# Performance work log

Hardware: AMD Instinct MI355X
Metric: run time of the kernel (lower is better)

Reference implementation:

```python
import jax, jax.numpy as jnp
import numpy as np

N_NODES = 100000
N_EDGES = 1600000
C = 64


def _spline_conv(x, src, dst, u, w, root, bias, n_nodes):
    """SplineConv, dim=1, kernel_size=2, degree=1, open spline, aggr='mean'.

    For K=2, degree=1, pseudo u in [0,1]: basis = (1-u) on knot 0, u on knot 1.
    message_e = (1-u_e) * x[src_e] @ w[0] + u_e * x[src_e] @ w[1]
    Compute the two GEMMs at node level (N < E) then gather, which is
    mathematically identical and cheaper.
    """
    h0 = x @ w[0]  # [N, C]
    h1 = x @ w[1]  # [N, C]
    uc = u[:, None]  # [E, 1]
    msg = (1.0 - uc) * h0[src] + uc * h1[src]  # [E, C]
    agg = jax.ops.segment_sum(msg, dst, num_segments=n_nodes)  # [N, C]
    deg = jax.ops.segment_sum(jnp.ones_like(u), dst, num_segments=n_nodes)
    agg = agg / jnp.maximum(deg, 1.0)[:, None]  # mean aggregation
    return agg + x @ root + bias


def setup_inputs() -> dict:
    key = jax.random.key(0)
    ks = jax.random.split(key, 10)
    x = jax.random.normal(ks[0], (N_NODES, C), dtype=jnp.float32)
    edge_index = jax.random.randint(ks[1], (2, N_EDGES), 0, N_NODES, dtype=jnp.int64)
    edge_attr = jax.random.uniform(ks[2], (N_EDGES, 1), dtype=jnp.float32)
    s = 1.0 / np.sqrt(C)
    w1 = jax.random.uniform(ks[3], (2, C, C), jnp.float32, -s, s)
    root1 = jax.random.uniform(ks[4], (C, C), jnp.float32, -s, s)
    b1 = jnp.zeros((C,), jnp.float32)
    w2 = jax.random.uniform(ks[5], (2, C, C), jnp.float32, -s, s)
    root2 = jax.random.uniform(ks[6], (C, C), jnp.float32, -s, s)
    b2 = jnp.zeros((C,), jnp.float32)
    return {"x": x, "edge_index": edge_index, "edge_attr": edge_attr,
            "w1": w1, "root1": root1, "b1": b1,
            "w2": w2, "root2": root2, "b2": b2}


def reference(x, edge_index, edge_attr, w1, root1, b1, w2, root2, b2):
    src, dst = edge_index[0], edge_index[1]
    u = edge_attr[:, 0]
    n = x.shape[0]
    h = _spline_conv(x, src, dst, u, w1, root1, b1, n)
    h = _spline_conv(h, src, dst, u, w2, root2, b2, n)
    return h
```

## Files before the change

### kernel.cpp

```cpp
#include <hip/hip_runtime.h>

#define CDIM 64

typedef __attribute__((ext_vector_type(8))) short bf16x8;
typedef __attribute__((ext_vector_type(4))) float f32x4;

__device__ __forceinline__ short bf16r(float f) {
    unsigned a = __float_as_uint(f);
    a = (a + 0x7fffu + ((a >> 16) & 1u)) >> 16;
    return (short)a;
}
__device__ __forceinline__ unsigned bfpack(float lo, float hi) {
    unsigned a = __float_as_uint(lo);
    a = (a + 0x7fffu + ((a >> 16) & 1u)) >> 16;
    unsigned b = __float_as_uint(hi);
    b = (b + 0x7fffu + ((b >> 16) & 1u)) & 0xffff0000u;
    return a | b;
}

__global__ __launch_bounds__(256) void k_pack(const float* __restrict__ x,
                                              unsigned* __restrict__ xb32, size_t n2) {
    size_t t = (size_t)blockIdx.x * 256 + threadIdx.x;
    size_t stride = (size_t)gridDim.x * 256;
    for (size_t i = t; i < n2; i += stride) {
        float2 v = ((const float2*)x)[i];
        xb32[i] = bfpack(v.x, v.y);
    }
}

#define NPB_SHIFT 9
#define BKN (1 << NPB_SHIFT)
#define BPAD 10240
#define PART_CH 2048

__global__ __launch_bounds__(256) void k_prep(int* __restrict__ bkt_cursor, int n_buckets,
                                              const float* __restrict__ w1,
                                              const float* __restrict__ root1,
                                              const float* __restrict__ w2,
                                              const float* __restrict__ root2,
                                              short* __restrict__ wtg) {
    int tid = threadIdx.x;
    if (blockIdx.x == 0) {
        if (tid < n_buckets) bkt_cursor[tid] = tid * BPAD;
        return;
    }
    int l = blockIdx.x - 1;
    const float* s0 = l ? w2 : w1;
    const float* srcs[3] = {s0, s0 + 4096, l ? root2 : root1};
    short* o = wtg + (size_t)l * 3 * 4096;
    for (int i = tid; i < 12288; i += 256) {
        int m = i >> 12, r = i & 4095, k = r >> 6, n = r & 63;
        o[(m << 12) + (n << 6) + k] = bf16r(srcs[m][r]);
    }
}

__global__ __launch_bounds__(256) void k_part(const int* __restrict__ src,
                                              const int* __restrict__ dst,
                                              const float* __restrict__ u,
                                              int* __restrict__ bkt_cursor,
                                              unsigned long long* __restrict__ rec,
                                              int n_edges, int n_buckets) {
    __shared__ int cnt_s[256];
    __shared__ int off_s[256];
    int tid = threadIdx.x;
    cnt_s[tid] = 0;
    __syncthreads();
    int e0 = blockIdx.x * PART_CH + tid * 8;
    int d[8], s[8];
    float uu[8];
    if (e0 + 8 <= n_edges) {
        int4 d0 = *(const int4*)(dst + e0), d1 = *(const int4*)(dst + e0 + 4);
        int4 s0 = *(const int4*)(src + e0), s1 = *(const int4*)(src + e0 + 4);
        float4 u0 = *(const float4*)(u + e0), u1 = *(const float4*)(u + e0 + 4);
        d[0]=d0.x; d[1]=d0.y; d[2]=d0.z; d[3]=d0.w; d[4]=d1.x; d[5]=d1.y; d[6]=d1.z; d[7]=d1.w;
        s[0]=s0.x; s[1]=s0.y; s[2]=s0.z; s[3]=s0.w; s[4]=s1.x; s[5]=s1.y; s[6]=s1.z; s[7]=s1.w;
        uu[0]=u0.x; uu[1]=u0.y; uu[2]=u0.z; uu[3]=u0.w; uu[4]=u1.x; uu[5]=u1.y; uu[6]=u1.z; uu[7]=u1.w;
    } else {
#pragma unroll
        for (int i = 0; i < 8; ++i) {
            int e = e0 + i;
            bool ok = e < n_edges;
            d[i] = ok ? dst[e] : -1;
            s[i] = ok ? src[e] : 0;
            uu[i] = ok ? u[e] : 0.f;
        }
    }
#pragma unroll
    for (int i = 0; i < 8; ++i)
        if (d[i] >= 0) atomicAdd(&cnt_s[d[i] >> NPB_SHIFT], 1);
    __syncthreads();
    if (tid < n_buckets) {
        int c = cnt_s[tid];
        off_s[tid] = c ? atomicAdd(&bkt_cursor[tid], c) : 0;
    }
    __syncthreads();
#pragma unroll
    for (int i = 0; i < 8; ++i) {
        if (d[i] >= 0) {
            int b = d[i] >> NPB_SHIFT;
            int p = atomicAdd(&off_s[b], 1);
            unsigned uq = (unsigned)(uu[i] * 32767.0f + 0.5f);
            rec[p] = ((unsigned long long)(unsigned)d[i] << 32)
                   | (unsigned long long)(((unsigned)s[i] << 15) | uq);
        }
    }
}

__global__ __launch_bounds__(256) void k_bscan(const int* __restrict__ bkt_cursor,
                                               int* __restrict__ ebase,
                                               int* __restrict__ row_start,
                                               int n_buckets, int n_nodes) {
    __shared__ int sm[256];
    int tid = threadIdx.x;
    int v = (tid < n_buckets) ? (bkt_cursor[tid] - tid * BPAD) : 0;
    sm[tid] = v;
    __syncthreads();
    for (int off = 1; off < 256; off <<= 1) {
        int t = (tid >= off) ? sm[tid - off] : 0;
        __syncthreads();
        sm[tid] += t;
        __syncthreads();
    }
    if (tid < n_buckets) ebase[tid] = sm[tid] - v;
    if (tid == 255) row_start[n_nodes] = sm[255];
}

__global__ __launch_bounds__(1024) void k_scat2(const unsigned long long* __restrict__ rec,
                                                const int* __restrict__ bkt_cursor,
                                                const int* __restrict__ ebase,
                                                int* __restrict__ row_start,
                                                unsigned* __restrict__ em32,
                                                int n_nodes) {
    __shared__ int cnt_s[BKN];
    __shared__ int sc_s[BKN];
    int tid = threadIdx.x;
    int b = blockIdx.x;
    int lo = b << NPB_SHIFT;
    int nrec = bkt_cursor[b] - b * BPAD;
    const unsigned long long* r0 = rec + (size_t)b * BPAD;
    int eb = ebase[b];

    if (tid < BKN) cnt_s[tid] = 0;
    __syncthreads();
    for (int i = tid; i < nrec; i += 1024) {
        int d = (int)(r0[i] >> 32) - lo;
        atomicAdd(&cnt_s[d], 1);
    }
    __syncthreads();
    if (tid < BKN) sc_s[tid] = cnt_s[tid];
    __syncthreads();
    for (int off = 1; off < BKN; off <<= 1) {
        int t = 0;
        if (tid < BKN && tid >= off) t = sc_s[tid - off];
        __syncthreads();
        if (tid < BKN) sc_s[tid] += t;
        __syncthreads();
    }
    if (tid < BKN) {
        int excl = sc_s[tid] - cnt_s[tid];
        int node = lo + tid;
        if (node < n_nodes) row_start[node] = eb + excl;
        cnt_s[tid] = excl;
    }
    __syncthreads();
    for (int i = tid; i < nrec; i += 1024) {
        unsigned long long r = r0[i];
        int d = (int)(r >> 32) - lo;
        int p = atomicAdd(&cnt_s[d], 1);
        em32[eb + p] = (unsigned)r;
    }
}

__global__ __launch_bounds__(256, 4) void k_fused(
        const unsigned* __restrict__ xb_in,
        const unsigned* __restrict__ em32,
        const int* __restrict__ row_start,
        const short* __restrict__ wb,
        const float* __restrict__ bias,
        float* __restrict__ out,
        unsigned short* __restrict__ xb_out,
        int n_nodes) {
    __shared__ __align__(16) unsigned gl[64][68];
    int wave = threadIdx.x >> 6;
    int lane = threadIdx.x & 63;
    int half = lane >> 5;
    int hl = lane & 31;
    int nodew = blockIdx.x * 64 + wave * 16;
    const float inv15 = 1.0f / 32767.0f;

    for (int t = 0; t < 16; ++t) {
        int n = nodew + t;
        if (n >= n_nodes) break;
        int start = row_start[n];
        int end = row_start[n + 1];
        float g0a = 0.f, g0b = 0.f, g1a = 0.f, g1b = 0.f;
        int j = start;
        for (; j + 8 <= end; j += 8) {
            unsigned e[4], v[4];
#pragma unroll
            for (int i = 0; i < 4; ++i) e[i] = em32[j + 2 * i + half];
#pragma unroll
            for (int i = 0; i < 4; ++i) v[i] = xb_in[(size_t)(e[i] >> 15) * 32 + hl];
#pragma unroll
            for (int i = 0; i < 4; ++i) {
                float uu = (float)(e[i] & 0x7fffu) * inv15;
                float c0 = __uint_as_float(v[i] << 16);
                float c1 = __uint_as_float(v[i] & 0xffff0000u);
                float wa = 1.0f - uu;
                g0a += wa * c0; g0b += wa * c1;
                g1a += uu * c0; g1b += uu * c1;
            }
        }
        if (j < end) {
            unsigned e[4], v[4];
            float m[4];
#pragma unroll
            for (int i = 0; i < 4; ++i) {
                int idx = j + 2 * i + half;
                bool ok = idx < end;
                e[i] = em32[ok ? idx : (end - 1)];
                m[i] = ok ? 1.0f : 0.0f;
            }
#pragma unroll
            for (int i = 0; i < 4; ++i) v[i] = xb_in[(size_t)(e[i] >> 15) * 32 + hl];
#pragma unroll
            for (int i = 0; i < 4; ++i) {
                float uu = (float)(e[i] & 0x7fffu) * inv15;
                float c0 = __uint_as_float(v[i] << 16);
                float c1 = __uint_as_float(v[i] & 0xffff0000u);
                float wa = (1.0f - uu) * m[i], wb2 = uu * m[i];
                g0a += wa * c0; g0b += wa * c1;
                g1a += wb2 * c0; g1b += wb2 * c1;
            }
        }
        g0a += __shfl_xor(g0a, 32);
        g0b += __shfl_xor(g0b, 32);
        g1a += __shfl_xor(g1a, 32);
        g1b += __shfl_xor(g1b, 32);
        float s = 1.0f / fmaxf((float)(end - start), 1.0f);
        if (half == 0) {
            gl[wave * 16 + t][hl] = bfpack(g0a * s, g0b * s);
            gl[wave * 16 + t][32 + hl] = bfpack(g1a * s, g1b * s);
        }
    }
    __syncthreads();

    int quad = lane >> 4;
    int m16 = lane & 15;
    int arow = nodew + m16;
    const short* gp = (const short*)&gl[wave * 16 + m16][0];
    const unsigned* xp = xb_in + (size_t)arow * 32;
    bf16x8 zf = {0, 0, 0, 0, 0, 0, 0, 0};
    bf16x8 aG0[2], aG1[2], aX[2];
#pragma unroll
    for (int kf = 0; kf < 2; ++kf) {
        aG0[kf] = *(const bf16x8*)(gp + kf * 32 + quad * 8);
        aG1[kf] = *(const bf16x8*)(gp + 64 + kf * 32 + quad * 8);
        aX[kf] = (arow < n_nodes) ? *(const bf16x8*)(xp + kf * 16 + quad * 4) : zf;
    }
#pragma unroll
    for (int nt = 0; nt < 4; ++nt) {
        f32x4 acc = {0.f, 0.f, 0.f, 0.f};
#pragma unroll
        for (int kf = 0; kf < 2; ++kf) {
            int col = nt * 16 + m16;
            bf16x8 b0 = *(const bf16x8*)(wb + (col << 6) + kf * 32 + quad * 8);
            bf16x8 b1 = *(const bf16x8*)(wb + ((64 + col) << 6) + kf * 32 + quad * 8);
            bf16x8 bR = *(const bf16x8*)(wb + ((128 + col) << 6) + kf * 32 + quad * 8);
            acc = __builtin_amdgcn_mfma_f32_16x16x32_bf16(aG0[kf], b0, acc, 0, 0, 0);
            acc = __builtin_amdgcn_mfma_f32_16x16x32_bf16(aG1[kf], b1, acc, 0, 0, 0);
            acc = __builtin_amdgcn_mfma_f32_16x16x32_bf16(aX[kf], bR, acc, 0, 0, 0);
        }
        float bcol = bias[nt * 16 + m16];
#pragma unroll
        for (int r = 0; r < 4; ++r) {
            int node = nodew + quad * 4 + r;
            if (node < n_nodes) {
                size_t off = (size_t)node * CDIM + nt * 16 + m16;
                float o = acc[r] + bcol;
                if (out) out[off] = o;
                if (xb_out) xb_out[off] = (unsigned short)bf16r(o);
            }
        }
    }
}

extern "C" void kernel_launch(void* const* d_in, const int* in_sizes, int n_in,
                              void* d_out, int out_size, void* d_ws, size_t ws_size,
                              hipStream_t stream) {
    const float* x = (const float*)d_in[0];
    const int* edge_index = (const int*)d_in[1];
    const float* edge_attr = (const float*)d_in[2];
    const float* w1 = (const float*)d_in[3];
    const float* root1 = (const float*)d_in[4];
    const float* b1 = (const float*)d_in[5];
    const float* w2 = (const float*)d_in[6];
    const float* root2 = (const float*)d_in[7];
    const float* b2 = (const float*)d_in[8];

    int n_nodes = in_sizes[0] / CDIM;
    int n_edges = in_sizes[2];
    const int* src = edge_index;
    const int* dst = edge_index + n_edges;

    size_t F = (size_t)n_nodes * CDIM;
    unsigned* xbA = (unsigned*)d_ws;
    unsigned* xbB = xbA + F / 2;
    unsigned* em32 = xbB + F / 2;
    int* row_start = (int*)(em32 + n_edges);
    int n_buckets = (n_nodes + BKN - 1) >> NPB_SHIFT;
    int* ebase = row_start + n_nodes + 1;
    int* bkt_cursor = ebase + n_buckets;
    uintptr_t p = (uintptr_t)(bkt_cursor + n_buckets);
    p = (p + 15) & ~(uintptr_t)15;
    short* wtg = (short*)p;
    p += (size_t)2 * 3 * 4096 * sizeof(short);
    p = (p + 15) & ~(uintptr_t)15;
    unsigned long long* rec = (unsigned long long*)p;
    float* out = (float*)d_out;

    int gB = (n_nodes + 63) / 64;
    int gP = (n_edges + PART_CH - 1) / PART_CH;

    k_pack<<<2048, 256, 0, stream>>>(x, xbA, F / 2);
    k_prep<<<3, 256, 0, stream>>>(bkt_cursor, n_buckets, w1, root1, w2, root2, wtg);
    k_part<<<gP, 256, 0, stream>>>(src, dst, edge_attr, bkt_cursor, rec, n_edges, n_buckets);
    k_bscan<<<1, 256, 0, stream>>>(bkt_cursor, ebase, row_start, n_buckets, n_nodes);
    k_scat2<<<n_buckets, 1024, 0, stream>>>(rec, bkt_cursor, ebase, row_start, em32, n_nodes);

    k_fused<<<gB, 256, 0, stream>>>(xbA, em32, row_start, wtg, b1,
                                    nullptr, (unsigned short*)xbB, n_nodes);
    k_fused<<<gB, 256, 0, stream>>>(xbB, em32, row_start, wtg + 3 * 4096, b2,
                                    out, nullptr, n_nodes);
}
```

Before: 293.5 us.

## Gather four nodes per wave with 16 lanes and 8-byte loads each

The edge-gather phase is remapped so each wave works on four nodes at once. Each node gets a 16-lane quarter-wave and each lane loads 8 bytes (four bf16 channels), where before 32-lane halves split one node's edges and had to be combined with cross-half shuffles. This roughly doubles the edges in flight per wave iteration, removes the shuffle reduction, and drops the block-wide __syncthreads, which is safe because each wave reads only its own LDS rows. The minimum-occupancy hint in launch bounds is also removed, so the compiler may use more registers. Costs: per-lane register use goes up, and nodes with different degrees inside the same wave can cause divergence.

New measurement: 268.3 us. -8.6%, faster.

```diff
diff --git a/kernel.cpp b/kernel.cpp
--- a/kernel.cpp
+++ b/kernel.cpp
@@ -171,7 +171,7 @@
     }
 }
 
-__global__ __launch_bounds__(256, 4) void k_fused(
+__global__ __launch_bounds__(256) void k_fused(
         const unsigned* __restrict__ xb_in,
         const unsigned* __restrict__ em32,
         const int* __restrict__ row_start,
@@ -183,67 +183,70 @@
     __shared__ __align__(16) unsigned gl[64][68];
     int wave = threadIdx.x >> 6;
     int lane = threadIdx.x & 63;
-    int half = lane >> 5;
-    int hl = lane & 31;
+    int q = lane >> 4;
+    int ql = lane & 15;
     int nodew = blockIdx.x * 64 + wave * 16;
     const float inv15 = 1.0f / 32767.0f;
 
-    for (int t = 0; t < 16; ++t) {
-        int n = nodew + t;
-        if (n >= n_nodes) break;
-        int start = row_start[n];
-        int end = row_start[n + 1];
-        float g0a = 0.f, g0b = 0.f, g1a = 0.f, g1b = 0.f;
+    for (int t = 0; t < 4; ++t) {
+        int n = nodew + q * 4 + t;
+        bool nok = n < n_nodes;
+        int start = nok ? row_start[n] : 0;
+        int end = nok ? row_start[n + 1] : 0;
+        float a0 = 0.f, a1 = 0.f, a2 = 0.f, a3 = 0.f;
+        float b0 = 0.f, b1 = 0.f, b2 = 0.f, b3 = 0.f;
         int j = start;
-        for (; j + 8 <= end; j += 8) {
-            unsigned e[4], v[4];
-#pragma unroll
-            for (int i = 0; i < 4; ++i) e[i] = em32[j + 2 * i + half];
-#pragma unroll
-            for (int i = 0; i < 4; ++i) v[i] = xb_in[(size_t)(e[i] >> 15) * 32 + hl];
+        for (; j + 4 <= end; j += 4) {
+            unsigned e[4];
+            uint2 v[4];
+#pragma unroll
+            for (int i = 0; i < 4; ++i) e[i] = em32[j + i];
+#pragma unroll
+            for (int i = 0; i < 4; ++i)
+                v[i] = *(const uint2*)(xb_in + (size_t)(e[i] >> 15) * 32 + 2 * ql);
 #pragma unroll
             for (int i = 0; i < 4; ++i) {
                 float uu = (float)(e[i] & 0x7fffu) * inv15;
-                float c0 = __uint_as_float(v[i] << 16);
-                float c1 = __uint_as_float(v[i] & 0xffff0000u);
                 float wa = 1.0f - uu;
-                g0a += wa * c0; g0b += wa * c1;
-                g1a += uu * c0; g1b += uu * c1;
+                float c0 = __uint_as_float(v[i].x << 16);
+                float c1 = __uint_as_float(v[i].x & 0xffff0000u);
+                float c2 = __uint_as_float(v[i].y << 16);
+                float c3 = __uint_as_float(v[i].y & 0xffff0000u);
+                a0 += wa * c0; a1 += wa * c1; a2 += wa * c2; a3 += wa * c3;
+                b0 += uu * c0; b1 += uu * c1; b2 += uu * c2; b3 += uu * c3;
             }
         }
         if (j < end) {
-            unsigned e[4], v[4];
+            unsigned e[4];
+            uint2 v[4];
             float m[4];
 #pragma unroll
             for (int i = 0; i < 4; ++i) {
-                int idx = j + 2 * i + half;
+                int idx = j + i;
                 bool ok = idx < end;
                 e[i] = em32[ok ? idx : (end - 1)];
                 m[i] = ok ? 1.0f : 0.0f;
             }
 #pragma unroll
-            for (int i = 0; i < 4; ++i) v[i] = xb_in[(size_t)(e[i] >> 15) * 32 + hl];
+            for (int i = 0; i < 4; ++i)
+                v[i] = *(const uint2*)(xb_in + (size_t)(e[i] >> 15) * 32 + 2 * ql);
 #pragma unroll
             for (int i = 0; i < 4; ++i) {
                 float uu = (float)(e[i] & 0x7fffu) * inv15;
-                float c0 = __uint_as_float(v[i] << 16);
-                float c1 = __uint_as_float(v[i] & 0xffff0000u);
-                float wa = (1.0f - uu) * m[i], wb2 = uu * m[i];
-                g0a += wa * c0; g0b += wa * c1;
-                g1a += wb2 * c0; g1b += wb2 * c1;
+                float wa = (1.0f - uu) * m[i], wu = uu * m[i];
+                float c0 = __uint_as_float(v[i].x << 16);
+                float c1 = __uint_as_float(v[i].x & 0xffff0000u);
+                float c2 = __uint_as_float(v[i].y << 16);
+                float c3 = __uint_as_float(v[i].y & 0xffff0000u);
+                a0 += wa * c0; a1 += wa * c1; a2 += wa * c2; a3 += wa * c3;
+                b0 += wu * c0; b1 += wu * c1; b2 += wu * c2; b3 += wu * c3;
             }
         }
-        g0a += __shfl_xor(g0a, 32);
-        g0b += __shfl_xor(g0b, 32);
-        g1a += __shfl_xor(g1a, 32);
-        g1b += __shfl_xor(g1b, 32);
         float s = 1.0f / fmaxf((float)(end - start), 1.0f);
-        if (half == 0) {
-            gl[wave * 16 + t][hl] = bfpack(g0a * s, g0b * s);
-            gl[wave * 16 + t][32 + hl] = bfpack(g1a * s, g1b * s);
-        }
-    }
-    __syncthreads();
+        int row = wave * 16 + q * 4 + t;
+        *(uint2*)&gl[row][2 * ql] = make_uint2(bfpack(a0 * s, a1 * s), bfpack(a2 * s, a3 * s));
+        *(uint2*)&gl[row][32 + 2 * ql] = make_uint2(bfpack(b0 * s, b1 * s), bfpack(b2 * s, b3 * s));
+    }
 
     int quad = lane >> 4;
     int m16 = lane & 15;
@@ -264,12 +267,12 @@
 #pragma unroll
         for (int kf = 0; kf < 2; ++kf) {
             int col = nt * 16 + m16;
-            bf16x8 b0 = *(const bf16x8*)(wb + (col << 6) + kf * 32 + quad * 8);
-            bf16x8 b1 = *(const bf16x8*)(wb + ((64 + col) << 6) + kf * 32 + quad * 8);
-            bf16x8 bR = *(const bf16x8*)(wb + ((128 + col) << 6) + kf * 32 + quad * 8);
-            acc = __builtin_amdgcn_mfma_f32_16x16x32_bf16(aG0[kf], b0, acc, 0, 0, 0);
-            acc = __builtin_amdgcn_mfma_f32_16x16x32_bf16(aG1[kf], b1, acc, 0, 0, 0);
-            acc = __builtin_amdgcn_mfma_f32_16x16x32_bf16(aX[kf], bR, acc, 0, 0, 0);
+            bf16x8 bw0 = *(const bf16x8*)(wb + (col << 6) + kf * 32 + quad * 8);
+            bf16x8 bw1 = *(const bf16x8*)(wb + ((64 + col) << 6) + kf * 32 + quad * 8);
+            bf16x8 bwR = *(const bf16x8*)(wb + ((128 + col) << 6) + kf * 32 + quad * 8);
+            acc = __builtin_amdgcn_mfma_f32_16x16x32_bf16(aG0[kf], bw0, acc, 0, 0, 0);
+            acc = __builtin_amdgcn_mfma_f32_16x16x32_bf16(aG1[kf], bw1, acc, 0, 0, 0);
+            acc = __builtin_amdgcn_mfma_f32_16x16x32_bf16(aX[kf], bwR, acc, 0, 0, 0);
         }
         float bcol = bias[nt * 16 + m16];
 #pragma unroll
```
